# Performance work log

Hardware: AMD Instinct MI355X
Metric: run time of the kernel (lower is better)

The kernel has to match this reference:

```python
import jax, jax.numpy as jnp
import numpy as np

H = 16
N_TASKS, N_DATA, N_DEV = 400_000, 200_000, 8


def _edges(key, n_src, n_dst, e):
    k1, k2 = jax.random.split(key)
    src = jax.random.randint(k1, (e,), 0, n_src)
    dst = jax.random.randint(k2, (e,), 0, n_dst)
    return jnp.stack([src, dst]).astype(jnp.int64)


def setup_inputs() -> dict:
    key = jax.random.key(0)
    ks = jax.random.split(key, 16)
    inp = {
        "x_tasks": jax.random.normal(ks[0], (N_TASKS, 12), jnp.float32),
        "x_data": jax.random.normal(ks[1], (N_DATA, 5), jnp.float32),
        "x_devices": jax.random.normal(ks[2], (N_DEV, 12), jnp.float32),
        "ei_data_tasks": _edges(ks[3], N_DATA, N_TASKS, 1_600_000),
        "ei_tasks_data": _edges(ks[4], N_TASKS, N_DATA, 1_600_000),
        "ei_tasks_devices": _edges(ks[5], N_TASKS, N_DEV, 400_000),
        "ei_devices_tasks": _edges(ks[6], N_DEV, N_TASKS, 400_000),
        "ei_data_devices": _edges(ks[7], N_DATA, N_DEV, 200_000),
        "ei_devices_data": _edges(ks[8], N_DEV, N_DATA, 200_000),
        "ei_tt_to": _edges(ks[9], N_TASKS, N_TASKS, 800_000),
        "ei_tt_from": _edges(ks[10], N_TASKS, N_TASKS, 800_000),
        # stacked GraphConv weights, grouped by input dim
        # W_rel5:  [0]=data->tasks, [1]=data->devices
        "W_rel5": jax.random.normal(ks[11], (2, 5, H), jnp.float32) * 0.3,
        # W_rel12: [0]=tasks->data,[1]=tasks->devices,[2]=devices->tasks,[3]=devices->data,[4]=tt_to,[5]=tt_from
        "W_rel12": jax.random.normal(ks[12], (6, 12, H), jnp.float32) * 0.2,
        # b_rel order: dt_t, t_d, t_dev, dev_t, d_dev, dev_d, tt_to, tt_from
        "b_rel": jax.random.normal(ks[13], (8, H), jnp.float32) * 0.1,
        # W_root5: [0]=tasks->data (dst data), [1]=devices->data
        "W_root5": jax.random.normal(ks[14], (2, 5, H), jnp.float32) * 0.3,
        # W_root12: [0]=data->tasks,[1]=tasks->devices,[2]=devices->tasks,[3]=data->devices,[4]=tt_to,[5]=tt_from
        "W_root12": jax.random.normal(ks[15], (6, 12, H), jnp.float32) * 0.2,
        # LayerNorm params: [0]=tasks, [1]=data, [2]=devices
        "ln_gamma": jnp.ones((3, H), jnp.float32),
        "ln_beta": jnp.zeros((3, H), jnp.float32),
    }
    return inp


def _graph_conv(x_src, x_dst, ei, W_rel, b_rel, W_root):
    # PyG GraphConv(aggr='add'): lin_rel(scatter_add(x_src[src] -> dst)) + lin_root(x_dst)
    agg = jax.ops.segment_sum(x_src[ei[0]], ei[1], num_segments=x_dst.shape[0])
    return agg @ W_rel + b_rel + x_dst @ W_root


def _layer_norm(x, gamma, beta, eps=1e-5):
    mu = jnp.mean(x, axis=-1, keepdims=True)
    var = jnp.mean(jnp.square(x - mu), axis=-1, keepdims=True)
    return (x - mu) * jax.lax.rsqrt(var + eps) * gamma + beta


def reference(x_tasks, x_data, x_devices,
              ei_data_tasks, ei_tasks_data, ei_tasks_devices, ei_devices_tasks,
              ei_data_devices, ei_devices_data, ei_tt_to, ei_tt_from,
              W_rel5, W_rel12, b_rel, W_root5, W_root12, ln_gamma, ln_beta):
    # HeteroConv(aggr='sum'): sum relation outputs per destination node type
    tasks = (
        _graph_conv(x_data, x_tasks, ei_data_tasks, W_rel5[0], b_rel[0], W_root12[0])
        + _graph_conv(x_devices, x_tasks, ei_devices_tasks, W_rel12[2], b_rel[3], W_root12[2])
        + _graph_conv(x_tasks, x_tasks, ei_tt_to, W_rel12[4], b_rel[6], W_root12[4])
        + _graph_conv(x_tasks, x_tasks, ei_tt_from, W_rel12[5], b_rel[7], W_root12[5])
    )
    data = (
        _graph_conv(x_tasks, x_data, ei_tasks_data, W_rel12[0], b_rel[1], W_root5[0])
        + _graph_conv(x_devices, x_data, ei_devices_data, W_rel12[3], b_rel[5], W_root5[1])
    )
    devices = (
        _graph_conv(x_tasks, x_devices, ei_tasks_devices, W_rel12[1], b_rel[2], W_root12[1])
        + _graph_conv(x_data, x_devices, ei_data_devices, W_rel5[1], b_rel[4], W_root12[3])
    )
    slope = 0.01
    tasks = jax.nn.leaky_relu(_layer_norm(tasks, ln_gamma[0], ln_beta[0]), slope)
    data = jax.nn.leaky_relu(_layer_norm(data, ln_gamma[1], ln_beta[1]), slope)
    devices = jax.nn.leaky_relu(_layer_norm(devices, ln_gamma[2], ln_beta[2]), slope)
    return tasks, data, devices
```

## Files before the change

### kernel.cpp

```cpp
#include <hip/hip_runtime.h>
#include <hip/hip_fp16.h>

#define LRELU(v) ((v) >= 0.0f ? (v) : 0.01f * (v))
#define EPB 8192
#define SHIFT 7
#define PAIRS 1600

struct PartDesc {
    const int* src; const int* dst;
    unsigned* part; int* cursor;
    int E, B, cap, chunk0;
};

struct PrepArgs {
    PartDesc r[6];
    int part_end;
    const int *tdev_e; int E_tdev; int sd12_b0, sd12_nb;
    const int *ddev_e; int E_ddev; int sd5_b0, sd5_nb;
    const float *x_tasks, *x_data, *x_dev;
    float *aggT_dev, *aggD_dev;
    __half *h_tasks; int NT; int ct_b0;
    __half *h_data;  int ND; int cd_b0;
};

template<int F>
__device__ __forceinline__ void loadrow(const float* __restrict__ x, unsigned s, float* v) {
    const float* p = x + (size_t)s * F;
    #pragma unroll
    for (int f = 0; f < F; ++f) v[f] = p[f];
}
template<>
__device__ __forceinline__ void loadrow<12>(const float* __restrict__ x, unsigned s, float* v) {
    const float4* p = (const float4*)(x + (size_t)s * 12);
    float4 a = p[0], b = p[1], c = p[2];
    v[0]=a.x; v[1]=a.y; v[2]=a.z; v[3]=a.w;
    v[4]=b.x; v[5]=b.y; v[6]=b.z; v[7]=b.w;
    v[8]=c.x; v[9]=c.y; v[10]=c.z; v[11]=c.w;
}

template<int F>
__device__ void scatter_dev_body(const float* __restrict__ x, const int* __restrict__ src,
                                 const int* __restrict__ dst, int E,
                                 float* __restrict__ agg, float* s_agg,
                                 int bl, int nb, int t)
{
    for (int i = t; i < 8 * F; i += 256) s_agg[i] = 0.0f;
    __syncthreads();
    const int stride = nb * 256;
    for (int e = bl * 256 + t; e < E; e += stride) {
        float v[F];
        loadrow<F>(x, (unsigned)src[e], v);
        int d = dst[e];
        #pragma unroll
        for (int f = 0; f < F; ++f) atomicAdd(&s_agg[d * F + f], v[f]);
    }
    __syncthreads();
    if (t < 8 * F) atomicAdd(&agg[t], s_agg[t]);
}

__global__ __launch_bounds__(256)
void prep_k(PrepArgs A)
{
    __shared__ unsigned shp[2 * PAIRS];
    const int bid = blockIdx.x;
    const int t = threadIdx.x;

    if (bid < A.part_end) {
        unsigned* hist = shp;
        unsigned* base = shp + PAIRS;
        int ri = 0;
        #pragma unroll
        for (int k = 1; k < 6; ++k) if (bid >= A.r[k].chunk0) ri = k;
        const PartDesc d = A.r[ri];
        const int e0 = (bid - d.chunk0) * EPB;
        const int e1 = min(d.E, e0 + EPB);
        const int npair = (d.B + 1) >> 1;

        for (int i = t; i < npair; i += 256) hist[i] = 0u;
        __syncthreads();
        for (int e = e0 + t; e < e1; e += 256) {
            int b = d.dst[e] >> SHIFT;
            atomicAdd(&hist[b >> 1], 1u << ((b & 1) << 4));
        }
        __syncthreads();
        for (int i = t; i < npair; i += 256) {
            unsigned h = hist[i];
            unsigned lo = h & 0xffffu, hi = h >> 16;
            unsigned blo = lo ? (unsigned)atomicAdd(&d.cursor[2 * i],     (int)lo) : 0u;
            unsigned bhi = hi ? (unsigned)atomicAdd(&d.cursor[2 * i + 1], (int)hi) : 0u;
            base[i] = (blo & 0xffffu) | (bhi << 16);
            hist[i] = 0u;
        }
        __syncthreads();
        for (int e = e0 + t; e < e1; e += 256) {
            int dd = d.dst[e];
            int b = dd >> SHIFT;
            unsigned s16 = (unsigned)(b & 1) << 4;
            unsigned r = atomicAdd(&hist[b >> 1], 1u << s16);
            unsigned idx = ((r >> s16) & 0xffffu) + ((base[b >> 1] >> s16) & 0xffffu);
            if ((int)idx < d.cap)
                d.part[(size_t)b * d.cap + idx] =
                    ((unsigned)d.src[e] << SHIFT) | ((unsigned)dd & 127u);
        }
    } else if (bid < A.sd5_b0) {
        scatter_dev_body<12>(A.x_tasks, A.tdev_e, A.tdev_e + A.E_tdev, A.E_tdev,
                             A.aggT_dev, (float*)shp, bid - A.sd12_b0, A.sd12_nb, t);
    } else if (bid < A.ct_b0) {
        scatter_dev_body<5>(A.x_data, A.ddev_e, A.ddev_e + A.E_ddev, A.E_ddev,
                            A.aggD_dev, (float*)shp, bid - A.sd5_b0, A.sd5_nb, t);
    } else if (bid < A.cd_b0) {
        int row = (bid - A.ct_b0) * 256 + t;
        if (row < A.NT) {
            const float* xr = A.x_tasks + (size_t)row * 12;
            __half h[16];
            #pragma unroll
            for (int j = 0; j < 12; ++j) h[j] = __float2half(xr[j]);
            #pragma unroll
            for (int j = 12; j < 16; ++j) h[j] = __half(0.0f);
            uint4* dst = (uint4*)(A.h_tasks + (size_t)row * 16);
            dst[0] = *(const uint4*)h;
            dst[1] = *(const uint4*)(h + 8);
        }
    } else {
        int row = (bid - A.cd_b0) * 256 + t;
        if (row < A.ND) {
            const float* xr = A.x_data + (size_t)row * 5;
            __half h[8];
            #pragma unroll
            for (int j = 0; j < 5; ++j) h[j] = __float2half(xr[j]);
            #pragma unroll
            for (int j = 5; j < 8; ++j) h[j] = __half(0.0f);
            *(uint4*)(A.h_data + (size_t)row * 8) = *(const uint4*)h;
        }
    }
}

struct LoadH8 {
    const __half* x;
    __device__ __forceinline__ void operator()(unsigned s, float* v) const {
        uint4 u = *(const uint4*)(x + (size_t)s * 8);
        const __half2* h = (const __half2*)&u;
        float2 f0 = __half22float2(h[0]);
        float2 f1 = __half22float2(h[1]);
        float2 f2 = __half22float2(h[2]);
        v[0] = f0.x; v[1] = f0.y; v[2] = f1.x; v[3] = f1.y; v[4] = f2.x;
    }
};
struct LoadH16 {
    const __half* x;
    __device__ __forceinline__ void operator()(unsigned s, float* v) const {
        const uint4* p = (const uint4*)(x + (size_t)s * 16);
        uint4 u0 = p[0], u1 = p[1];
        const __half2* a = (const __half2*)&u0;
        const __half2* b = (const __half2*)&u1;
        float2 f;
        f = __half22float2(a[0]); v[0] = f.x; v[1] = f.y;
        f = __half22float2(a[1]); v[2] = f.x; v[3] = f.y;
        f = __half22float2(a[2]); v[4] = f.x; v[5] = f.y;
        f = __half22float2(a[3]); v[6] = f.x; v[7] = f.y;
        f = __half22float2(b[0]); v[8] = f.x; v[9] = f.y;
        f = __half22float2(b[1]); v[10] = f.x; v[11] = f.y;
    }
};
struct LoadF12 {
    const float* x;
    __device__ __forceinline__ void operator()(unsigned s, float* v) const {
        loadrow<12>(x, s, v);
    }
};

template<int F>
__device__ __forceinline__ void addrow(float* a, const float* v) {
    #pragma unroll
    for (int f = 0; f < F; ++f) atomicAdd(a + f, v[f]);
}

template<int F, class LD>
__device__ __forceinline__
void agg_rel4(const unsigned* __restrict__ p, int cnt, LD ld, float* acc, int t)
{
    int i = 4 * t;
    for (; i + 3 < cnt; i += 1024) {
        uint4 e = *(const uint4*)(p + i);
        float v0[F], v1[F], v2[F], v3[F];
        ld(e.x >> SHIFT, v0);
        ld(e.y >> SHIFT, v1);
        ld(e.z >> SHIFT, v2);
        ld(e.w >> SHIFT, v3);
        addrow<F>(acc + (e.x & 127u) * F, v0);
        addrow<F>(acc + (e.y & 127u) * F, v1);
        addrow<F>(acc + (e.z & 127u) * F, v2);
        addrow<F>(acc + (e.w & 127u) * F, v3);
    }
    const int jend = min(i + 4, cnt);
    for (int j = i; j < jend; ++j) {
        unsigned e = p[j];
        float v[F];
        ld(e >> SHIFT, v);
        addrow<F>(acc + (e & 127u) * F, v);
    }
}

struct AggDesc { const unsigned* part; const int* cursor; int cap, b0; };
struct AggArgs {
    AggDesc r[6];
    const __half *h_tasks, *h_data; const float* x_dev;
    __half *aD_t, *aDev_t, *aTo, *aFrom, *aT_d, *aDev_d;
    int NT, ND;
};

template<int F, int OSTR, class LD>
__device__ __forceinline__
void agg_body(const unsigned* p, int cnt, LD ld, float* acc,
              __half* out, int N, int n0, int t)
{
    const int nn = min(128, N - n0);
    for (int i = t; i < 128 * F; i += 256) acc[i] = 0.0f;
    __syncthreads();
    agg_rel4<F>(p, cnt, ld, acc, t);
    __syncthreads();
    __half* o = out + (size_t)n0 * OSTR;
    for (int i = t; i < nn * OSTR; i += 256) {
        int n = i / OSTR, c = i - n * OSTR;
        float v = (c < F) ? acc[n * F + c] : 0.0f;
        o[i] = __float2half(v);
    }
}

__global__ __launch_bounds__(256, 6)
void agg_k(AggArgs A)
{
    __shared__ float acc[128 * 12];
    const int bid = blockIdx.x;
    const int t = threadIdx.x;
    int ri = 0;
    #pragma unroll
    for (int k = 1; k < 6; ++k) if (bid >= A.r[k].b0) ri = k;
    const AggDesc d = A.r[ri];
    const int b = bid - d.b0;
    const unsigned* p = d.part + (size_t)b * d.cap;
    const int cnt = min(d.cursor[b], d.cap);
    const int n0 = b << SHIFT;

    if (ri == 0)      agg_body<5, 6 >(p, cnt, LoadH8 {A.h_data},  acc, A.aD_t,   A.NT, n0, t);
    else if (ri == 1) agg_body<12, 12>(p, cnt, LoadF12{A.x_dev},   acc, A.aDev_t, A.NT, n0, t);
    else if (ri == 2) agg_body<12, 12>(p, cnt, LoadH16{A.h_tasks}, acc, A.aTo,    A.NT, n0, t);
    else if (ri == 3) agg_body<12, 12>(p, cnt, LoadH16{A.h_tasks}, acc, A.aFrom,  A.NT, n0, t);
    else if (ri == 4) agg_body<12, 12>(p, cnt, LoadH16{A.h_tasks}, acc, A.aT_d,   A.ND, n0, t);
    else              agg_body<12, 12>(p, cnt, LoadF12{A.x_dev},   acc, A.aDev_d, A.ND, n0, t);
}

__device__ __forceinline__ float2 upk(unsigned u) {
    __half2 h = *(__half2*)&u; return __half22float2(h);
}
__device__ __forceinline__ void load12h(const __half* base, size_t i, float* f) {
    const uint2* q = (const uint2*)(base + i * 12);
    uint2 u0 = q[0], u1 = q[1], u2 = q[2];
    float2 x;
    x = upk(u0.x); f[0]  = x.x; f[1]  = x.y;
    x = upk(u0.y); f[2]  = x.x; f[3]  = x.y;
    x = upk(u1.x); f[4]  = x.x; f[5]  = x.y;
    x = upk(u1.y); f[6]  = x.x; f[7]  = x.y;
    x = upk(u2.x); f[8]  = x.x; f[9]  = x.y;
    x = upk(u2.y); f[10] = x.x; f[11] = x.y;
}

template<int NF>
__device__ __forceinline__
void dot_ln_store(const float* __restrict__ f, const float* __restrict__ sW,
                  const float* __restrict__ sb, const float* __restrict__ sg,
                  const float* __restrict__ sbt, float* __restrict__ op)
{
    float o[16];
    #pragma unroll
    for (int k = 0; k < 16; ++k) o[k] = sb[k];
    const float4* w4 = (const float4*)sW;
    #pragma unroll
    for (int j = 0; j < NF; ++j) {
        const float fj = f[j];
        float4 w0 = w4[j*4+0], w1 = w4[j*4+1], w2 = w4[j*4+2], w3 = w4[j*4+3];
        o[0] =fmaf(fj,w0.x,o[0]);  o[1] =fmaf(fj,w0.y,o[1]);
        o[2] =fmaf(fj,w0.z,o[2]);  o[3] =fmaf(fj,w0.w,o[3]);
        o[4] =fmaf(fj,w1.x,o[4]);  o[5] =fmaf(fj,w1.y,o[5]);
        o[6] =fmaf(fj,w1.z,o[6]);  o[7] =fmaf(fj,w1.w,o[7]);
        o[8] =fmaf(fj,w2.x,o[8]);  o[9] =fmaf(fj,w2.y,o[9]);
        o[10]=fmaf(fj,w2.z,o[10]); o[11]=fmaf(fj,w2.w,o[11]);
        o[12]=fmaf(fj,w3.x,o[12]); o[13]=fmaf(fj,w3.y,o[13]);
        o[14]=fmaf(fj,w3.z,o[14]); o[15]=fmaf(fj,w3.w,o[15]);
    }
    float mu = 0.0f;
    #pragma unroll
    for (int k = 0; k < 16; ++k) mu += o[k];
    mu *= 0.0625f;
    float var = 0.0f;
    #pragma unroll
    for (int k = 0; k < 16; ++k) { float d = o[k] - mu; var = fmaf(d, d, var); }
    var *= 0.0625f;
    const float r = rsqrtf(var + 1e-5f);
    #pragma unroll
    for (int k = 0; k < 16; ++k) {
        float v = (o[k] - mu) * r * sg[k] + sbt[k];
        op[k] = LRELU(v);
    }
}

struct FinArgs {
    const __half *aD_t, *aDev_t, *aTo, *aFrom, *aT_d, *aDev_d;
    const float *x_tasks, *x_data, *x_dev;
    const float *aggT_dev, *aggD_dev;
    const float *W_rel5, *W_rel12, *b_rel, *W_root5, *W_root12, *ln_g, *ln_b;
    float *out_tasks, *out_data, *out_dev;
    int NT, ND, NDEV, Bt, Bd;
};

__global__ __launch_bounds__(256, 4)
void finalize_k(FinArgs A)
{
    __shared__ __align__(16) float lds[896];
    const int bid = blockIdx.x;
    const int t = threadIdx.x;

    if (bid < A.Bt) {
        float* sW = lds; float* sb = lds + 848; float* sg = lds + 864; float* sbt = lds + 880;
        for (int i = t; i < 80; i += 256) sW[i] = A.W_rel5[i];
        for (int i = t; i < 192; i += 256) {
            sW[80  + i] = A.W_rel12[384 + i];
            sW[272 + i] = A.W_rel12[768 + i];
            sW[464 + i] = A.W_rel12[960 + i];
            sW[656 + i] = A.W_root12[i] + A.W_root12[384 + i]
                        + A.W_root12[768 + i] + A.W_root12[960 + i];
        }
        if (t < 16) {
            sb[t]  = A.b_rel[t] + A.b_rel[48 + t] + A.b_rel[96 + t] + A.b_rel[112 + t];
            sg[t]  = A.ln_g[t];
            sbt[t] = A.ln_b[t];
        }
        __syncthreads();
        const int i = bid * 256 + t;
        if (i < A.NT) {
            float f[53];
            {
                const unsigned* q = (const unsigned*)A.aD_t + (size_t)i * 3;
                unsigned u0 = q[0], u1 = q[1], u2 = q[2];
                float2 a = upk(u0), b = upk(u1), c = upk(u2);
                f[0] = a.x; f[1] = a.y; f[2] = b.x; f[3] = b.y; f[4] = c.x;
            }
            load12h(A.aDev_t, i, f + 5);
            load12h(A.aTo,   i, f + 17);
            load12h(A.aFrom, i, f + 29);
            const float4* xr = (const float4*)(A.x_tasks + (size_t)i * 12);
            float4 x0 = xr[0], x1 = xr[1], x2 = xr[2];
            f[41]=x0.x; f[42]=x0.y; f[43]=x0.z; f[44]=x0.w;
            f[45]=x1.x; f[46]=x1.y; f[47]=x1.z; f[48]=x1.w;
            f[49]=x2.x; f[50]=x2.y; f[51]=x2.z; f[52]=x2.w;
            dot_ln_store<53>(f, sW, sb, sg, sbt, A.out_tasks + (size_t)i * 16);
        }
    } else if (bid < A.Bt + A.Bd) {
        float* sW = lds; float* sb = lds + 464; float* sg = lds + 480; float* sbt = lds + 496;
        for (int i = t; i < 192; i += 256) {
            sW[i]       = A.W_rel12[i];
            sW[192 + i] = A.W_rel12[576 + i];
        }
        for (int i = t; i < 80; i += 256)
            sW[384 + i] = A.W_root5[i] + A.W_root5[80 + i];
        if (t < 16) {
            sb[t]  = A.b_rel[16 + t] + A.b_rel[80 + t];
            sg[t]  = A.ln_g[16 + t];
            sbt[t] = A.ln_b[16 + t];
        }
        __syncthreads();
        const int i = (bid - A.Bt) * 256 + t;
        if (i < A.ND) {
            float f[29];
            load12h(A.aT_d,   i, f);
            load12h(A.aDev_d, i, f + 12);
            const float* xr = A.x_data + (size_t)i * 5;
            #pragma unroll
            for (int j = 0; j < 5; ++j) f[24 + j] = xr[j];
            dot_ln_store<29>(f, sW, sb, sg, sbt, A.out_data + (size_t)i * 16);
        }
    } else {
        const int i = t;
        if (i < A.NDEV) {
            float acc[16];
            #pragma unroll
            for (int k = 0; k < 16; ++k) acc[k] = A.b_rel[32 + k] + A.b_rel[64 + k];
            #pragma unroll
            for (int j = 0; j < 12; ++j) {
                float fj = A.aggT_dev[i * 12 + j];
                #pragma unroll
                for (int k = 0; k < 16; ++k) acc[k] = fmaf(fj, A.W_rel12[192 + j * 16 + k], acc[k]);
            }
            #pragma unroll
            for (int j = 0; j < 5; ++j) {
                float fj = A.aggD_dev[i * 5 + j];
                #pragma unroll
                for (int k = 0; k < 16; ++k) acc[k] = fmaf(fj, A.W_rel5[80 + j * 16 + k], acc[k]);
            }
            #pragma unroll
            for (int j = 0; j < 12; ++j) {
                float fj = A.x_dev[i * 12 + j];
                #pragma unroll
                for (int k = 0; k < 16; ++k)
                    acc[k] = fmaf(fj, A.W_root12[192 + j * 16 + k] + A.W_root12[576 + j * 16 + k], acc[k]);
            }
            float mu = 0.0f;
            #pragma unroll
            for (int k = 0; k < 16; ++k) mu += acc[k];
            mu *= 0.0625f;
            float var = 0.0f;
            #pragma unroll
            for (int k = 0; k < 16; ++k) { float d = acc[k] - mu; var = fmaf(d, d, var); }
            var *= 0.0625f;
            const float r = rsqrtf(var + 1e-5f);
            #pragma unroll
            for (int k = 0; k < 16; ++k) {
                float v = (acc[k] - mu) * r * A.ln_g[32 + k] + A.ln_b[32 + k];
                A.out_dev[i * 16 + k] = LRELU(v);
            }
        }
    }
}

extern "C" void kernel_launch(void* const* d_in, const int* in_sizes, int n_in,
                              void* d_out, int out_size, void* d_ws, size_t ws_size,
                              hipStream_t stream)
{
    const float* x_tasks = (const float*)d_in[0];
    const float* x_data  = (const float*)d_in[1];
    const float* x_dev   = (const float*)d_in[2];
    const int* ei_dt    = (const int*)d_in[3];
    const int* ei_td    = (const int*)d_in[4];
    const int* ei_tdev  = (const int*)d_in[5];
    const int* ei_devt  = (const int*)d_in[6];
    const int* ei_ddev  = (const int*)d_in[7];
    const int* ei_devd  = (const int*)d_in[8];
    const int* ei_to    = (const int*)d_in[9];
    const int* ei_from  = (const int*)d_in[10];
    const float* W_rel5   = (const float*)d_in[11];
    const float* W_rel12  = (const float*)d_in[12];
    const float* b_rel    = (const float*)d_in[13];
    const float* W_root5  = (const float*)d_in[14];
    const float* W_root12 = (const float*)d_in[15];
    const float* ln_g     = (const float*)d_in[16];
    const float* ln_b     = (const float*)d_in[17];

    const int NT   = in_sizes[0] / 12;
    const int ND   = in_sizes[1] / 5;
    const int NDEV = in_sizes[2] / 12;
    const int E_dt   = in_sizes[3]  / 2;
    const int E_td   = in_sizes[4]  / 2;
    const int E_tdev = in_sizes[5]  / 2;
    const int E_devt = in_sizes[6]  / 2;
    const int E_ddev = in_sizes[7]  / 2;
    const int E_devd = in_sizes[8]  / 2;
    const int E_to   = in_sizes[9]  / 2;
    const int E_from = in_sizes[10] / 2;

    const int B_t = (NT + 127) / 128;
    const int B_d = (ND + 127) / 128;

    auto capf = [](int E, int B) {
        int mean = E / B + 1;
        int c = mean + mean / 4 + 128;
        return (c + 3) & ~3;
    };
    const int cap_dt   = capf(E_dt,   B_t);
    const int cap_devt = capf(E_devt, B_t);
    const int cap_to   = capf(E_to,   B_t);
    const int cap_from = capf(E_from, B_t);
    const int cap_td   = capf(E_td,   B_d);
    const int cap_devd = capf(E_devd, B_d);

    float* ws = (float*)d_ws;
    size_t o = 0;
    int* c_dt   = (int*)(ws + o); o += 3200;
    int* c_devt = (int*)(ws + o); o += 3200;
    int* c_to   = (int*)(ws + o); o += 3200;
    int* c_from = (int*)(ws + o); o += 3200;
    int* c_td   = (int*)(ws + o); o += 1600;
    int* c_devd = (int*)(ws + o); o += 1600;
    float* aggT_dev = ws + o; o += 96;
    float* aggD_dev = ws + o; o += 48;
    const size_t zero_bytes = o * sizeof(float);
    o = (o + 3) & ~(size_t)3;
    __half* h_tasks = (__half*)(ws + o); o += (size_t)NT * 8;
    __half* h_data  = (__half*)(ws + o); o += (size_t)ND * 4;
    __half* aD_t    = (__half*)(ws + o); o += (size_t)NT * 3;
    __half* aDev_t  = (__half*)(ws + o); o += (size_t)NT * 6;
    __half* aTo     = (__half*)(ws + o); o += (size_t)NT * 6;
    __half* aFrom   = (__half*)(ws + o); o += (size_t)NT * 6;
    __half* aT_d    = (__half*)(ws + o); o += (size_t)ND * 6;
    __half* aDev_d  = (__half*)(ws + o); o += (size_t)ND * 6;
    unsigned* p_dt   = (unsigned*)(ws + o); o += (size_t)B_t * cap_dt;
    unsigned* p_devt = (unsigned*)(ws + o); o += (size_t)B_t * cap_devt;
    unsigned* p_to   = (unsigned*)(ws + o); o += (size_t)B_t * cap_to;
    unsigned* p_from = (unsigned*)(ws + o); o += (size_t)B_t * cap_from;
    unsigned* p_td   = (unsigned*)(ws + o); o += (size_t)B_d * cap_td;
    unsigned* p_devd = (unsigned*)(ws + o); o += (size_t)B_d * cap_devd;

    hipMemsetAsync(d_ws, 0, zero_bytes, stream);

    auto nc = [](int e) { return (e + EPB - 1) / EPB; };
    PrepArgs pa;
    int ch = 0;
    pa.r[0] = { ei_dt,   ei_dt   + E_dt,   p_dt,   c_dt,   E_dt,   B_t, cap_dt,   ch }; ch += nc(E_dt);
    pa.r[1] = { ei_devt, ei_devt + E_devt, p_devt, c_devt, E_devt, B_t, cap_devt, ch }; ch += nc(E_devt);
    pa.r[2] = { ei_to,   ei_to   + E_to,   p_to,   c_to,   E_to,   B_t, cap_to,   ch }; ch += nc(E_to);
    pa.r[3] = { ei_from, ei_from + E_from, p_from, c_from, E_from, B_t, cap_from, ch }; ch += nc(E_from);
    pa.r[4] = { ei_td,   ei_td   + E_td,   p_td,   c_td,   E_td,   B_d, cap_td,   ch }; ch += nc(E_td);
    pa.r[5] = { ei_devd, ei_devd + E_devd, p_devd, c_devd, E_devd, B_d, cap_devd, ch }; ch += nc(E_devd);
    pa.part_end = ch;
    pa.tdev_e = ei_tdev; pa.E_tdev = E_tdev; pa.sd12_b0 = ch; pa.sd12_nb = 192; ch += 192;
    pa.ddev_e = ei_ddev; pa.E_ddev = E_ddev; pa.sd5_b0  = ch; pa.sd5_nb  = 96;  ch += 96;
    pa.x_tasks = x_tasks; pa.x_data = x_data; pa.x_dev = x_dev;
    pa.aggT_dev = aggT_dev; pa.aggD_dev = aggD_dev;
    pa.h_tasks = h_tasks; pa.NT = NT; pa.ct_b0 = ch; ch += (NT + 255) / 256;
    pa.h_data  = h_data;  pa.ND = ND; pa.cd_b0 = ch; ch += (ND + 255) / 256;

    prep_k<<<ch, 256, 0, stream>>>(pa);

    AggArgs aa;
    int ab = 0;
    aa.r[0] = { p_dt,   c_dt,   cap_dt,   ab }; ab += B_t;
    aa.r[1] = { p_devt, c_devt, cap_devt, ab }; ab += B_t;
    aa.r[2] = { p_to,   c_to,   cap_to,   ab }; ab += B_t;
    aa.r[3] = { p_from, c_from, cap_from, ab }; ab += B_t;
    aa.r[4] = { p_td,   c_td,   cap_td,   ab }; ab += B_d;
    aa.r[5] = { p_devd, c_devd, cap_devd, ab }; ab += B_d;
    aa.h_tasks = h_tasks; aa.h_data = h_data; aa.x_dev = x_dev;
    aa.aD_t = aD_t; aa.aDev_t = aDev_t; aa.aTo = aTo; aa.aFrom = aFrom;
    aa.aT_d = aT_d; aa.aDev_d = aDev_d;
    aa.NT = NT; aa.ND = ND;

    agg_k<<<ab, 256, 0, stream>>>(aa);

    float* out_tasks = (float*)d_out;
    float* out_data  = out_tasks + (size_t)NT * 16;
    float* out_dev   = out_data  + (size_t)ND * 16;

    FinArgs fa;
    fa.aD_t = aD_t; fa.aDev_t = aDev_t; fa.aTo = aTo; fa.aFrom = aFrom;
    fa.aT_d = aT_d; fa.aDev_d = aDev_d;
    fa.x_tasks = x_tasks; fa.x_data = x_data; fa.x_dev = x_dev;
    fa.aggT_dev = aggT_dev; fa.aggD_dev = aggD_dev;
    fa.W_rel5 = W_rel5; fa.W_rel12 = W_rel12; fa.b_rel = b_rel;
    fa.W_root5 = W_root5; fa.W_root12 = W_root12; fa.ln_g = ln_g; fa.ln_b = ln_b;
    fa.out_tasks = out_tasks; fa.out_data = out_data; fa.out_dev = out_dev;
    fa.NT = NT; fa.ND = ND; fa.NDEV = NDEV;
    fa.Bt = (NT + 255) / 256; fa.Bd = (ND + 255) / 256;

    finalize_k<<<fa.Bt + fa.Bd + 1, 256, 0, stream>>>(fa);
}
```

Measured before the change: 633.5 us.

## Fuse per-relation aggregation with finalize into one kernel via shared memory

Result: faster. 610.0 us (-3.7%).

```diff
diff --git a/kernel.cpp b/kernel.cpp
--- a/kernel.cpp
+++ b/kernel.cpp
@@ -169,125 +169,49 @@
     }
 };
 
-template<int F>
-__device__ __forceinline__ void addrow(float* a, const float* v) {
-    #pragma unroll
-    for (int f = 0; f < F; ++f) atomicAdd(a + f, v[f]);
-}
-
-template<int F, class LD>
+template<int F, int STR, class LD>
 __device__ __forceinline__
-void agg_rel4(const unsigned* __restrict__ p, int cnt, LD ld, float* acc, int t)
-{
-    int i = 4 * t;
-    for (; i + 3 < cnt; i += 1024) {
-        uint4 e = *(const uint4*)(p + i);
-        float v0[F], v1[F], v2[F], v3[F];
-        ld(e.x >> SHIFT, v0);
-        ld(e.y >> SHIFT, v1);
-        ld(e.z >> SHIFT, v2);
-        ld(e.w >> SHIFT, v3);
-        addrow<F>(acc + (e.x & 127u) * F, v0);
-        addrow<F>(acc + (e.y & 127u) * F, v1);
-        addrow<F>(acc + (e.z & 127u) * F, v2);
-        addrow<F>(acc + (e.w & 127u) * F, v3);
-    }
-    const int jend = min(i + 4, cnt);
-    for (int j = i; j < jend; ++j) {
-        unsigned e = p[j];
+void agg_rel(const unsigned* __restrict__ p, int cnt, LD ld, float* __restrict__ acc, int t)
+{
+    int i = t;
+    for (; i + 256 < cnt; i += 512) {
+        unsigned e0 = p[i], e1 = p[i + 256];
+        float v0[F], v1[F];
+        ld(e0 >> SHIFT, v0);
+        ld(e1 >> SHIFT, v1);
+        float* a0 = acc + (e0 & 127u) * STR;
+        float* a1 = acc + (e1 & 127u) * STR;
+        #pragma unroll
+        for (int f = 0; f < F; ++f) atomicAdd(a0 + f, v0[f]);
+        #pragma unroll
+        for (int f = 0; f < F; ++f) atomicAdd(a1 + f, v1[f]);
+    }
+    if (i < cnt) {
+        unsigned e = p[i];
         float v[F];
         ld(e >> SHIFT, v);
-        addrow<F>(acc + (e & 127u) * F, v);
-    }
-}
-
-struct AggDesc { const unsigned* part; const int* cursor; int cap, b0; };
-struct AggArgs {
-    AggDesc r[6];
-    const __half *h_tasks, *h_data; const float* x_dev;
-    __half *aD_t, *aDev_t, *aTo, *aFrom, *aT_d, *aDev_d;
-    int NT, ND;
-};
-
-template<int F, int OSTR, class LD>
+        float* a = acc + (e & 127u) * STR;
+        #pragma unroll
+        for (int f = 0; f < F; ++f) atomicAdd(a + f, v[f]);
+    }
+}
+
+__device__ __forceinline__ void fma16(float* o, float fj, const float4* __restrict__ w) {
+    float4 w0 = w[0], w1 = w[1], w2 = w[2], w3 = w[3];
+    o[0] =fmaf(fj,w0.x,o[0]);  o[1] =fmaf(fj,w0.y,o[1]);
+    o[2] =fmaf(fj,w0.z,o[2]);  o[3] =fmaf(fj,w0.w,o[3]);
+    o[4] =fmaf(fj,w1.x,o[4]);  o[5] =fmaf(fj,w1.y,o[5]);
+    o[6] =fmaf(fj,w1.z,o[6]);  o[7] =fmaf(fj,w1.w,o[7]);
+    o[8] =fmaf(fj,w2.x,o[8]);  o[9] =fmaf(fj,w2.y,o[9]);
+    o[10]=fmaf(fj,w2.z,o[10]); o[11]=fmaf(fj,w2.w,o[11]);
+    o[12]=fmaf(fj,w3.x,o[12]); o[13]=fmaf(fj,w3.y,o[13]);
+    o[14]=fmaf(fj,w3.z,o[14]); o[15]=fmaf(fj,w3.w,o[15]);
+}
+
 __device__ __forceinline__
-void agg_body(const unsigned* p, int cnt, LD ld, float* acc,
-              __half* out, int N, int n0, int t)
-{
-    const int nn = min(128, N - n0);
-    for (int i = t; i < 128 * F; i += 256) acc[i] = 0.0f;
-    __syncthreads();
-    agg_rel4<F>(p, cnt, ld, acc, t);
-    __syncthreads();
-    __half* o = out + (size_t)n0 * OSTR;
-    for (int i = t; i < nn * OSTR; i += 256) {
-        int n = i / OSTR, c = i - n * OSTR;
-        float v = (c < F) ? acc[n * F + c] : 0.0f;
-        o[i] = __float2half(v);
-    }
-}
-
-__global__ __launch_bounds__(256, 6)
-void agg_k(AggArgs A)
-{
-    __shared__ float acc[128 * 12];
-    const int bid = blockIdx.x;
-    const int t = threadIdx.x;
-    int ri = 0;
-    #pragma unroll
-    for (int k = 1; k < 6; ++k) if (bid >= A.r[k].b0) ri = k;
-    const AggDesc d = A.r[ri];
-    const int b = bid - d.b0;
-    const unsigned* p = d.part + (size_t)b * d.cap;
-    const int cnt = min(d.cursor[b], d.cap);
-    const int n0 = b << SHIFT;
-
-    if (ri == 0)      agg_body<5, 6 >(p, cnt, LoadH8 {A.h_data},  acc, A.aD_t,   A.NT, n0, t);
-    else if (ri == 1) agg_body<12, 12>(p, cnt, LoadF12{A.x_dev},   acc, A.aDev_t, A.NT, n0, t);
-    else if (ri == 2) agg_body<12, 12>(p, cnt, LoadH16{A.h_tasks}, acc, A.aTo,    A.NT, n0, t);
-    else if (ri == 3) agg_body<12, 12>(p, cnt, LoadH16{A.h_tasks}, acc, A.aFrom,  A.NT, n0, t);
-    else if (ri == 4) agg_body<12, 12>(p, cnt, LoadH16{A.h_tasks}, acc, A.aT_d,   A.ND, n0, t);
-    else              agg_body<12, 12>(p, cnt, LoadF12{A.x_dev},   acc, A.aDev_d, A.ND, n0, t);
-}
-
-__device__ __forceinline__ float2 upk(unsigned u) {
-    __half2 h = *(__half2*)&u; return __half22float2(h);
-}
-__device__ __forceinline__ void load12h(const __half* base, size_t i, float* f) {
-    const uint2* q = (const uint2*)(base + i * 12);
-    uint2 u0 = q[0], u1 = q[1], u2 = q[2];
-    float2 x;
-    x = upk(u0.x); f[0]  = x.x; f[1]  = x.y;
-    x = upk(u0.y); f[2]  = x.x; f[3]  = x.y;
-    x = upk(u1.x); f[4]  = x.x; f[5]  = x.y;
-    x = upk(u1.y); f[6]  = x.x; f[7]  = x.y;
-    x = upk(u2.x); f[8]  = x.x; f[9]  = x.y;
-    x = upk(u2.y); f[10] = x.x; f[11] = x.y;
-}
-
-template<int NF>
-__device__ __forceinline__
-void dot_ln_store(const float* __restrict__ f, const float* __restrict__ sW,
-                  const float* __restrict__ sb, const float* __restrict__ sg,
-                  const float* __restrict__ sbt, float* __restrict__ op)
-{
-    float o[16];
-    #pragma unroll
-    for (int k = 0; k < 16; ++k) o[k] = sb[k];
-    const float4* w4 = (const float4*)sW;
-    #pragma unroll
-    for (int j = 0; j < NF; ++j) {
-        const float fj = f[j];
-        float4 w0 = w4[j*4+0], w1 = w4[j*4+1], w2 = w4[j*4+2], w3 = w4[j*4+3];
-        o[0] =fmaf(fj,w0.x,o[0]);  o[1] =fmaf(fj,w0.y,o[1]);
-        o[2] =fmaf(fj,w0.z,o[2]);  o[3] =fmaf(fj,w0.w,o[3]);
-        o[4] =fmaf(fj,w1.x,o[4]);  o[5] =fmaf(fj,w1.y,o[5]);
-        o[6] =fmaf(fj,w1.z,o[6]);  o[7] =fmaf(fj,w1.w,o[7]);
-        o[8] =fmaf(fj,w2.x,o[8]);  o[9] =fmaf(fj,w2.y,o[9]);
-        o[10]=fmaf(fj,w2.z,o[10]); o[11]=fmaf(fj,w2.w,o[11]);
-        o[12]=fmaf(fj,w3.x,o[12]); o[13]=fmaf(fj,w3.y,o[13]);
-        o[14]=fmaf(fj,w3.z,o[14]); o[15]=fmaf(fj,w3.w,o[15]);
-    }
+void ln_store(float* o, const float* __restrict__ sg, const float* __restrict__ sbt,
+              float* __restrict__ op)
+{
     float mu = 0.0f;
     #pragma unroll
     for (int k = 0; k < 16; ++k) mu += o[k];
@@ -300,28 +224,40 @@
     #pragma unroll
     for (int k = 0; k < 16; ++k) {
         float v = (o[k] - mu) * r * sg[k] + sbt[k];
-        op[k] = LRELU(v);
-    }
-}
-
-struct FinArgs {
-    const __half *aD_t, *aDev_t, *aTo, *aFrom, *aT_d, *aDev_d;
-    const float *x_tasks, *x_data, *x_dev;
+        o[k] = LRELU(v);
+    }
+    float4* q = (float4*)op;
+    const float4* s = (const float4*)o;
+    q[0] = s[0]; q[1] = s[1]; q[2] = s[2]; q[3] = s[3];
+}
+
+struct FusedDesc { const unsigned* part; const int* cursor; int cap; };
+struct FusedArgs {
+    FusedDesc rt[4];
+    FusedDesc rd[2];
+    const __half *h_tasks, *h_data;
+    const float *x_dev, *x_tasks, *x_data;
     const float *aggT_dev, *aggD_dev;
     const float *W_rel5, *W_rel12, *b_rel, *W_root5, *W_root12, *ln_g, *ln_b;
     float *out_tasks, *out_data, *out_dev;
     int NT, ND, NDEV, Bt, Bd;
 };
 
-__global__ __launch_bounds__(256, 4)
-void finalize_k(FinArgs A)
-{
-    __shared__ __align__(16) float lds[896];
+__global__ __launch_bounds__(256, 6)
+void fused_k(FusedArgs A)
+{
+    __shared__ __align__(16) float lds[6144];
     const int bid = blockIdx.x;
     const int t = threadIdx.x;
 
     if (bid < A.Bt) {
-        float* sW = lds; float* sb = lds + 848; float* sg = lds + 864; float* sbt = lds + 880;
+        float* acc = lds;
+        float* sW  = lds + 5248;
+        float* sb  = lds + 6096;
+        float* sg  = lds + 6112;
+        float* sbt = lds + 6128;
+
+        for (int i = t; i < 5248; i += 256) acc[i] = 0.0f;
         for (int i = t; i < 80; i += 256) sW[i] = A.W_rel5[i];
         for (int i = t; i < 192; i += 256) {
             sW[80  + i] = A.W_rel12[384 + i];
@@ -336,27 +272,48 @@
             sbt[t] = A.ln_b[t];
         }
         __syncthreads();
-        const int i = bid * 256 + t;
-        if (i < A.NT) {
-            float f[53];
-            {
-                const unsigned* q = (const unsigned*)A.aD_t + (size_t)i * 3;
-                unsigned u0 = q[0], u1 = q[1], u2 = q[2];
-                float2 a = upk(u0), b = upk(u1), c = upk(u2);
-                f[0] = a.x; f[1] = a.y; f[2] = b.x; f[3] = b.y; f[4] = c.x;
+
+        const int b = bid;
+        { const FusedDesc d = A.rt[0];
+          agg_rel<5, 41>(d.part + (size_t)b * d.cap, min(d.cursor[b], d.cap),
+                         LoadH8{A.h_data}, acc + 0, t); }
+        { const FusedDesc d = A.rt[1];
+          agg_rel<12, 41>(d.part + (size_t)b * d.cap, min(d.cursor[b], d.cap),
+                          LoadF12{A.x_dev}, acc + 5, t); }
+        { const FusedDesc d = A.rt[2];
+          agg_rel<12, 41>(d.part + (size_t)b * d.cap, min(d.cursor[b], d.cap),
+                          LoadH16{A.h_tasks}, acc + 17, t); }
+        { const FusedDesc d = A.rt[3];
+          agg_rel<12, 41>(d.part + (size_t)b * d.cap, min(d.cursor[b], d.cap),
+                          LoadH16{A.h_tasks}, acc + 29, t); }
+        __syncthreads();
+
+        if (t < 128) {
+            const int i = (bid << SHIFT) + t;
+            if (i < A.NT) {
+                const float4* xr = (const float4*)(A.x_tasks + (size_t)i * 12);
+                float4 x0 = xr[0], x1 = xr[1], x2 = xr[2];
+                float o[16];
+                #pragma unroll
+                for (int k = 0; k < 16; ++k) o[k] = sb[k];
+                const float4* w4 = (const float4*)sW;
+                const float* ar = acc + t * 41;
+                #pragma unroll
+                for (int j = 0; j < 41; ++j) fma16(o, ar[j], w4 + 4 * j);
+                float xf[12] = {x0.x,x0.y,x0.z,x0.w, x1.x,x1.y,x1.z,x1.w, x2.x,x2.y,x2.z,x2.w};
+                #pragma unroll
+                for (int j = 0; j < 12; ++j) fma16(o, xf[j], w4 + 4 * (41 + j));
+                ln_store(o, sg, sbt, A.out_tasks + (size_t)i * 16);
             }
-            load12h(A.aDev_t, i, f + 5);
-            load12h(A.aTo,   i, f + 17);
-            load12h(A.aFrom, i, f + 29);
-            const float4* xr = (const float4*)(A.x_tasks + (size_t)i * 12);
-            float4 x0 = xr[0], x1 = xr[1], x2 = xr[2];
-            f[41]=x0.x; f[42]=x0.y; f[43]=x0.z; f[44]=x0.w;
-            f[45]=x1.x; f[46]=x1.y; f[47]=x1.z; f[48]=x1.w;
-            f[49]=x2.x; f[50]=x2.y; f[51]=x2.z; f[52]=x2.w;
-            dot_ln_store<53>(f, sW, sb, sg, sbt, A.out_tasks + (size_t)i * 16);
         }
     } else if (bid < A.Bt + A.Bd) {
-        float* sW = lds; float* sb = lds + 464; float* sg = lds + 480; float* sbt = lds + 496;
+        float* acc = lds;
+        float* sW  = lds + 3200;
+        float* sb  = lds + 3664;
+        float* sg  = lds + 3680;
+        float* sbt = lds + 3696;
+
+        for (int i = t; i < 3200; i += 256) acc[i] = 0.0f;
         for (int i = t; i < 192; i += 256) {
             sW[i]       = A.W_rel12[i];
             sW[192 + i] = A.W_rel12[576 + i];
@@ -369,55 +326,58 @@
             sbt[t] = A.ln_b[16 + t];
         }
         __syncthreads();
-        const int i = (bid - A.Bt) * 256 + t;
-        if (i < A.ND) {
-            float f[29];
-            load12h(A.aT_d,   i, f);
-            load12h(A.aDev_d, i, f + 12);
-            const float* xr = A.x_data + (size_t)i * 5;
-            #pragma unroll
-            for (int j = 0; j < 5; ++j) f[24 + j] = xr[j];
-            dot_ln_store<29>(f, sW, sb, sg, sbt, A.out_data + (size_t)i * 16);
+
+        const int b = bid - A.Bt;
+        { const FusedDesc d = A.rd[0];
+          agg_rel<12, 25>(d.part + (size_t)b * d.cap, min(d.cursor[b], d.cap),
+                          LoadH16{A.h_tasks}, acc + 0, t); }
+        { const FusedDesc d = A.rd[1];
+          agg_rel<12, 25>(d.part + (size_t)b * d.cap, min(d.cursor[b], d.cap),
+                          LoadF12{A.x_dev}, acc + 12, t); }
+        __syncthreads();
+
+        if (t < 128) {
+            const int i = (b << SHIFT) + t;
+            if (i < A.ND) {
+                const float* xr = A.x_data + (size_t)i * 5;
+                float o[16];
+                #pragma unroll
+                for (int k = 0; k < 16; ++k) o[k] = sb[k];
+                const float4* w4 = (const float4*)sW;
+                const float* ar = acc + t * 25;
+                #pragma unroll
+                for (int j = 0; j < 24; ++j) fma16(o, ar[j], w4 + 4 * j);
+                #pragma unroll
+                for (int j = 0; j < 5; ++j) fma16(o, xr[j], w4 + 4 * (24 + j));
+                ln_store(o, sg, sbt, A.out_data + (size_t)i * 16);
+            }
         }
     } else {
         const int i = t;
         if (i < A.NDEV) {
-            float acc[16];
-            #pragma unroll
-            for (int k = 0; k < 16; ++k) acc[k] = A.b_rel[32 + k] + A.b_rel[64 + k];
+            float o[16];
+            #pragma unroll
+            for (int k = 0; k < 16; ++k) o[k] = A.b_rel[32 + k] + A.b_rel[64 + k];
             #pragma unroll
             for (int j = 0; j < 12; ++j) {
                 float fj = A.aggT_dev[i * 12 + j];
                 #pragma unroll
-                for (int k = 0; k < 16; ++k) acc[k] = fmaf(fj, A.W_rel12[192 + j * 16 + k], acc[k]);
+                for (int k = 0; k < 16; ++k) o[k] = fmaf(fj, A.W_rel12[192 + j * 16 + k], o[k]);
             }
             #pragma unroll
             for (int j = 0; j < 5; ++j) {
                 float fj = A.aggD_dev[i * 5 + j];
                 #pragma unroll
-                for (int k = 0; k < 16; ++k) acc[k] = fmaf(fj, A.W_rel5[80 + j * 16 + k], acc[k]);
+                for (int k = 0; k < 16; ++k) o[k] = fmaf(fj, A.W_rel5[80 + j * 16 + k], o[k]);
             }
             #pragma unroll
             for (int j = 0; j < 12; ++j) {
                 float fj = A.x_dev[i * 12 + j];
                 #pragma unroll
                 for (int k = 0; k < 16; ++k)
-                    acc[k] = fmaf(fj, A.W_root12[192 + j * 16 + k] + A.W_root12[576 + j * 16 + k], acc[k]);
+                    o[k] = fmaf(fj, A.W_root12[192 + j * 16 + k] + A.W_root12[576 + j * 16 + k], o[k]);
             }
-            float mu = 0.0f;
-            #pragma unroll
-            for (int k = 0; k < 16; ++k) mu += acc[k];
-            mu *= 0.0625f;
-            float var = 0.0f;
-            #pragma unroll
-            for (int k = 0; k < 16; ++k) { float d = acc[k] - mu; var = fmaf(d, d, var); }
-            var *= 0.0625f;
-            const float r = rsqrtf(var + 1e-5f);
-            #pragma unroll
-            for (int k = 0; k < 16; ++k) {
-                float v = (acc[k] - mu) * r * A.ln_g[32 + k] + A.ln_b[32 + k];
-                A.out_dev[i * 16 + k] = LRELU(v);
-            }
+            ln_store(o, A.ln_g + 32, A.ln_b + 32, A.out_dev + (size_t)i * 16);
         }
     }
 }
@@ -486,12 +446,6 @@
     o = (o + 3) & ~(size_t)3;
     __half* h_tasks = (__half*)(ws + o); o += (size_t)NT * 8;
     __half* h_data  = (__half*)(ws + o); o += (size_t)ND * 4;
-    __half* aD_t    = (__half*)(ws + o); o += (size_t)NT * 3;
-    __half* aDev_t  = (__half*)(ws + o); o += (size_t)NT * 6;
-    __half* aTo     = (__half*)(ws + o); o += (size_t)NT * 6;
-    __half* aFrom   = (__half*)(ws + o); o += (size_t)NT * 6;
-    __half* aT_d    = (__half*)(ws + o); o += (size_t)ND * 6;
-    __half* aDev_d  = (__half*)(ws + o); o += (size_t)ND * 6;
     unsigned* p_dt   = (unsigned*)(ws + o); o += (size_t)B_t * cap_dt;
     unsigned* p_devt = (unsigned*)(ws + o); o += (size_t)B_t * cap_devt;
     unsigned* p_to   = (unsigned*)(ws + o); o += (size_t)B_t * cap_to;
@@ -520,35 +474,25 @@
 
     prep_k<<<ch, 256, 0, stream>>>(pa);
 
-    AggArgs aa;
-    int ab = 0;
-    aa.r[0] = { p_dt,   c_dt,   cap_dt,   ab }; ab += B_t;
-    aa.r[1] = { p_devt, c_devt, cap_devt, ab }; ab += B_t;
-    aa.r[2] = { p_to,   c_to,   cap_to,   ab }; ab += B_t;
-    aa.r[3] = { p_from, c_from, cap_from, ab }; ab += B_t;
-    aa.r[4] = { p_td,   c_td,   cap_td,   ab }; ab += B_d;
-    aa.r[5] = { p_devd, c_devd, cap_devd, ab }; ab += B_d;
-    aa.h_tasks = h_tasks; aa.h_data = h_data; aa.x_dev = x_dev;
-    aa.aD_t = aD_t; aa.aDev_t = aDev_t; aa.aTo = aTo; aa.aFrom = aFrom;
-    aa.aT_d = aT_d; aa.aDev_d = aDev_d;
-    aa.NT = NT; aa.ND = ND;
-
-    agg_k<<<ab, 256, 0, stream>>>(aa);
-
     float* out_tasks = (float*)d_out;
     float* out_data  = out_tasks + (size_t)NT * 16;
     float* out_dev   = out_data  + (size_t)ND * 16;
 
-    FinArgs fa;
-    fa.aD_t = aD_t; fa.aDev_t = aDev_t; fa.aTo = aTo; fa.aFrom = aFrom;
-    fa.aT_d = aT_d; fa.aDev_d = aDev_d;
-    fa.x_tasks = x_tasks; fa.x_data = x_data; fa.x_dev = x_dev;
+    FusedArgs fa;
+    fa.rt[0] = { p_dt,   c_dt,   cap_dt   };
+    fa.rt[1] = { p_devt, c_devt, cap_devt };
+    fa.rt[2] = { p_to,   c_to,   cap_to   };
+    fa.rt[3] = { p_from, c_from, cap_from };
+    fa.rd[0] = { p_td,   c_td,   cap_td   };
+    fa.rd[1] = { p_devd, c_devd, cap_devd };
+    fa.h_tasks = h_tasks; fa.h_data = h_data;
+    fa.x_dev = x_dev; fa.x_tasks = x_tasks; fa.x_data = x_data;
     fa.aggT_dev = aggT_dev; fa.aggD_dev = aggD_dev;
     fa.W_rel5 = W_rel5; fa.W_rel12 = W_rel12; fa.b_rel = b_rel;
     fa.W_root5 = W_root5; fa.W_root12 = W_root12; fa.ln_g = ln_g; fa.ln_b = ln_b;
     fa.out_tasks = out_tasks; fa.out_data = out_data; fa.out_dev = out_dev;
     fa.NT = NT; fa.ND = ND; fa.NDEV = NDEV;
-    fa.Bt = (NT + 255) / 256; fa.Bd = (ND + 255) / 256;
-
-    finalize_k<<<fa.Bt + fa.Bd + 1, 256, 0, stream>>>(fa);
-}
+    fa.Bt = B_t; fa.Bd = B_d;
+
+    fused_k<<<B_t + B_d + 1, 256, 0, stream>>>(fa);
+}
```
